# Kernel tuning notes

Hardware: AMD Instinct MI355X
Metric: run time of the kernel (lower is better)

The kernel has to match this reference:

```python
import jax, jax.numpy as jnp
import numpy as np

BATCH, SEQ, IN_DIM, OUT_DIM = 8, 512, 32, 1
D_MODEL, N_LAYERS = 512, 4
D_INNER = 2 * D_MODEL          # expand_factor=2
D_STATE = 16
D_CONV = 4
DT_RANK = (D_MODEL + 15) // 16  # ceil(d_model/16) = 32


def setup_inputs() -> dict:
    key = jax.random.key(0)
    ks = iter(jax.random.split(key, 24))
    def w(shape, fan_in):
        return jax.random.normal(next(ks), shape, jnp.float32) * (fan_in ** -0.5)
    dt = jax.random.uniform(next(ks), (N_LAYERS, D_INNER), jnp.float32, 1e-3, 0.1)
    A_log = jnp.broadcast_to(jnp.log(jnp.arange(1, D_STATE + 1, dtype=jnp.float32)),
                             (N_LAYERS, D_INNER, D_STATE)) * 1.0
    return {
        "x": jax.random.normal(next(ks), (BATCH, SEQ, IN_DIM), jnp.float32),
        "enc_w": w((D_MODEL, IN_DIM), IN_DIM),
        "enc_b": jnp.zeros((D_MODEL,), jnp.float32),
        "in_proj_w": w((N_LAYERS, 2 * D_INNER, D_MODEL), D_MODEL),
        "conv_w": w((N_LAYERS, D_INNER, 1, D_CONV), D_CONV),
        "conv_b": jnp.zeros((N_LAYERS, D_INNER), jnp.float32),
        "x_proj_w": w((N_LAYERS, DT_RANK + 2 * D_STATE, D_INNER), D_INNER),
        "dt_proj_w": w((N_LAYERS, D_INNER, DT_RANK), DT_RANK),
        "dt_proj_b": jnp.log(jnp.expm1(dt)),  # inverse softplus init
        "A_log": A_log,
        "D": jnp.ones((N_LAYERS, D_INNER), jnp.float32),
        "out_proj_w": w((N_LAYERS, D_MODEL, D_INNER), D_INNER),
        "norm_w": jnp.ones((N_LAYERS, D_MODEL), jnp.float32),
        "dec_w1": w((D_MODEL // 2, D_MODEL), D_MODEL),
        "dec_b1": jnp.zeros((D_MODEL // 2,), jnp.float32),
        "dec_w2": w((OUT_DIM, D_MODEL // 2), D_MODEL // 2),
        "dec_b2": jnp.zeros((OUT_DIM,), jnp.float32),
    }


def _rmsnorm(x, w, eps=1e-5):
    return x * jax.lax.rsqrt(jnp.mean(x * x, axis=-1, keepdims=True) + eps) * w


def _mixer(x, in_w, cw, cb, xp_w, dtp_w, dtp_b, A_log, Dp, out_w):
    B, L, _ = x.shape
    xz = x @ in_w.T                               # (B,L,2*di)
    xr, z = jnp.split(xz, 2, axis=-1)
    # causal depthwise conv1d (cross-correlation, left pad d_conv-1)
    xc = jax.lax.conv_general_dilated(
        xr.transpose(0, 2, 1), cw, window_strides=(1,),
        padding=[(D_CONV - 1, 0)], feature_group_count=D_INNER,
        dimension_numbers=("NCW", "OIW", "NCW"))    # (B,di,L)
    xr = jax.nn.silu(xc.transpose(0, 2, 1) + cb)   # (B,L,di)
    dbc = xr @ xp_w.T                              # (B,L,dt_rank+2N)
    delta = jax.nn.softplus(dbc[..., :DT_RANK] @ dtp_w.T + dtp_b)  # (B,L,di)
    Bm = dbc[..., DT_RANK:DT_RANK + D_STATE]       # (B,L,N)
    Cm = dbc[..., DT_RANK + D_STATE:]              # (B,L,N)
    A = -jnp.exp(A_log)                            # (di,N)
    dA = jnp.exp(delta[..., None] * A)             # (B,L,di,N)
    dBx = delta[..., None] * Bm[:, :, None, :] * xr[..., None]
    def step(h, inputs):
        dA_t, dBx_t = inputs
        h = dA_t * h + dBx_t
        return h, h
    h0 = jnp.zeros((B, D_INNER, D_STATE), xr.dtype)
    _, hs = jax.lax.scan(step, h0, (dA.transpose(1, 0, 2, 3), dBx.transpose(1, 0, 2, 3)))
    y = jnp.einsum("lbdn,bln->bld", hs, Cm) + Dp * xr
    y = y * jax.nn.silu(z)
    return y @ out_w.T


def reference(x, enc_w, enc_b, in_proj_w, conv_w, conv_b, x_proj_w, dt_proj_w,
              dt_proj_b, A_log, D, out_proj_w, norm_w, dec_w1, dec_b1, dec_w2, dec_b2):
    h = x @ enc_w.T + enc_b
    for i in range(in_proj_w.shape[0]):   # residual pre-norm Mamba blocks
        h = h + _mixer(_rmsnorm(h, norm_w[i]), in_proj_w[i], conv_w[i], conv_b[i],
                       x_proj_w[i], dt_proj_w[i], dt_proj_b[i], A_log[i], D[i],
                       out_proj_w[i])
    h = h[:, -1, :]
    h = jax.nn.relu(h @ dec_w1.T + dec_b1)
    return (h @ dec_w2.T + dec_b2).reshape(-1)
```

## Files before the change

### kernel.cpp

```cpp
#include <hip/hip_runtime.h>
#include <math.h>

#define BATCH   8
#define SEQ     512
#define IN_DIM  32
#define D_MODEL 512
#define N_LAYERS 4
#define D_INNER 1024
#define D_STATE 16
#define D_CONV  4
#define DT_RANK 32
#define NTOK    (BATCH * SEQ)
#define BLK_T   32
#define NCHUNK  (SEQ / BLK_T)

typedef __attribute__((ext_vector_type(8))) short short8_t;
typedef __attribute__((ext_vector_type(4))) float floatx4;

__device__ __forceinline__ float sigmoidf_(float x) { return 1.f / (1.f + __expf(-x)); }

__device__ __forceinline__ unsigned short f2bf(float f) {
    unsigned int u = __float_as_uint(f);
    return (unsigned short)((u + 0x7fffu + ((u >> 16) & 1u)) >> 16);
}
__device__ __forceinline__ float bf2f(unsigned short u) {
    return __uint_as_float((unsigned int)u << 16);
}

__global__ __launch_bounds__(256) void cast_all_kernel(
    const float* __restrict__ a, unsigned short* __restrict__ oa, int qa,
    const float* __restrict__ b, unsigned short* __restrict__ ob, int qb,
    const float* __restrict__ c, unsigned short* __restrict__ oc, int qc)
{
    int v = blockIdx.x * 256 + threadIdx.x;
    const float* in; unsigned short* out;
    if (v < qa)                { in = a; out = oa; }
    else if (v < qa + qb)      { v -= qa; in = b; out = ob; }
    else if (v < qa + qb + qc) { v -= qa + qb; in = c; out = oc; }
    else return;
    const float4 x = *(const float4*)&in[v * 4];
    ushort4 o;
    o.x = f2bf(x.x); o.y = f2bf(x.y); o.z = f2bf(x.z); o.w = f2bf(x.w);
    *(ushort4*)&out[v * 4] = o;
}

template<int BM, int BN, bool OUTBF, bool ILV>
__global__ __launch_bounds__(256) void gemm_mfma(
    const unsigned short* __restrict__ A, int lda,
    const unsigned short* __restrict__ W, int ldw,
    const float* __restrict__ R,
    void* __restrict__ Cv, int ldc,
    int K)
{
    constexpr int MT = BM / 32;
    constexpr int NT = BN / 32;
    constexpr int SA = BM / 64;
    constexpr int SB = BN / 64;
    __shared__ __align__(16) unsigned short sA[BM * 32];
    __shared__ __align__(16) unsigned short sB[BN * 32];

    const int tid  = threadIdx.x;
    const int lane = tid & 63;
    const int wave = tid >> 6;
    const int wm0  = (wave >> 1) * (BM / 2);
    const int wn0  = (wave & 1) * (BN / 2);
    const int lrow = lane & 15;
    const int m0 = blockIdx.y * BM;
    const int n0 = blockIdx.x * BN;

    const unsigned short* aptr[SA];
    const unsigned short* bptr[SB];
    #pragma unroll
    for (int s = 0; s < SA; ++s) {
        const int r = wave * (BM / 4) + s * 16 + (lane >> 2);
        const int cc = (((lane & 3) ^ ((r >> 1) & 3))) * 8;
        aptr[s] = &A[(size_t)(m0 + r) * lda + cc];
    }
    #pragma unroll
    for (int s = 0; s < SB; ++s) {
        const int r = wave * (BN / 4) + s * 16 + (lane >> 2);
        const int cc = (((lane & 3) ^ ((r >> 1) & 3))) * 8;
        bptr[s] = &W[(size_t)(n0 + r) * ldw + cc];
    }
    int aoff[MT], boff[NT];
    #pragma unroll
    for (int mt = 0; mt < MT; ++mt) {
        const int m = wm0 + mt * 16 + lrow;
        aoff[mt] = m * 32 + (((lane >> 4) ^ ((m >> 1) & 3)) * 8);
    }
    #pragma unroll
    for (int nt = 0; nt < NT; ++nt) {
        const int n = wn0 + nt * 16 + lrow;
        boff[nt] = n * 32 + (((lane >> 4) ^ ((n >> 1) & 3)) * 8);
    }

    floatx4 acc[MT][NT];
    #pragma unroll
    for (int mt = 0; mt < MT; ++mt)
        #pragma unroll
        for (int nt = 0; nt < NT; ++nt)
            acc[mt][nt] = (floatx4){0.f, 0.f, 0.f, 0.f};

    for (int k0 = 0; k0 < K; k0 += 32) {
        #pragma unroll
        for (int s = 0; s < SA; ++s)
            __builtin_amdgcn_global_load_lds(
                (const __attribute__((address_space(1))) void*)(aptr[s] + k0),
                (__attribute__((address_space(3))) void*)&sA[(wave * (BM / 4) + s * 16) * 32],
                16, 0, 0);
        #pragma unroll
        for (int s = 0; s < SB; ++s)
            __builtin_amdgcn_global_load_lds(
                (const __attribute__((address_space(1))) void*)(bptr[s] + k0),
                (__attribute__((address_space(3))) void*)&sB[(wave * (BN / 4) + s * 16) * 32],
                16, 0, 0);
        __syncthreads();
        short8_t af[MT], bfr[NT];
        #pragma unroll
        for (int mt = 0; mt < MT; ++mt)
            af[mt] = *(const short8_t*)&sA[aoff[mt]];
        #pragma unroll
        for (int nt = 0; nt < NT; ++nt)
            bfr[nt] = *(const short8_t*)&sB[boff[nt]];
        #pragma unroll
        for (int mt = 0; mt < MT; ++mt)
            #pragma unroll
            for (int nt = 0; nt < NT; ++nt)
                acc[mt][nt] = __builtin_amdgcn_mfma_f32_16x16x32_bf16(af[mt], bfr[nt], acc[mt][nt], 0, 0, 0);
        __syncthreads();
    }

    #pragma unroll
    for (int mt = 0; mt < MT; ++mt) {
        const int mbase = m0 + wm0 + mt * 16 + (lane >> 4) * 4;
        #pragma unroll
        for (int nt = 0; nt < NT; ++nt) {
            const int n = n0 + wn0 + nt * 16 + (lane & 15);
            int np = n;
            if (ILV) np = (n < 32) ? n : ((n < 48) ? 32 + 2 * (n - 32) : 33 + 2 * (n - 48));
            #pragma unroll
            for (int r = 0; r < 4; ++r) {
                float v = acc[mt][nt][r];
                if (OUTBF) {
                    ((unsigned short*)Cv)[(size_t)(mbase + r) * ldc + np] = f2bf(v);
                } else {
                    if (R) v += R[(size_t)(mbase + r) * ldc + np];
                    ((float*)Cv)[(size_t)(mbase + r) * ldc + np] = v;
                }
            }
        }
    }
}

template<bool SOFTPLUS>
__global__ __launch_bounds__(256) void gemm_bt64(
    const float* __restrict__ A, int lda,
    const float* __restrict__ W,
    const float* __restrict__ bias,
    float* __restrict__ C,
    int N, int K, int ldc)
{
    __shared__ __align__(16) float As[16][64];
    __shared__ __align__(16) float Ws[16][64];
    const int tid = threadIdx.x;
    const int tx = tid & 15, ty = tid >> 4;
    const int m0 = blockIdx.y * 64, n0 = blockIdx.x * 64;
    const int lm = tid >> 2;
    const int lk = (tid & 3) * 4;

    float acc[4][4] = {};
    for (int k0 = 0; k0 < K; k0 += 16) {
        float4 av = *(const float4*)&A[(size_t)(m0 + lm) * lda + k0 + lk];
        float4 wv = *(const float4*)&W[(size_t)(n0 + lm) * K   + k0 + lk];
        As[lk + 0][lm] = av.x; As[lk + 1][lm] = av.y; As[lk + 2][lm] = av.z; As[lk + 3][lm] = av.w;
        Ws[lk + 0][lm] = wv.x; Ws[lk + 1][lm] = wv.y; Ws[lk + 2][lm] = wv.z; Ws[lk + 3][lm] = wv.w;
        __syncthreads();
        #pragma unroll
        for (int k = 0; k < 16; ++k) {
            float4 a4 = *(const float4*)&As[k][ty * 4];
            float4 b4 = *(const float4*)&Ws[k][tx * 4];
            float a[4] = {a4.x, a4.y, a4.z, a4.w};
            float b[4] = {b4.x, b4.y, b4.z, b4.w};
            #pragma unroll
            for (int i = 0; i < 4; ++i)
                #pragma unroll
                for (int j = 0; j < 4; ++j)
                    acc[i][j] = fmaf(a[i], b[j], acc[i][j]);
        }
        __syncthreads();
    }
    #pragma unroll
    for (int i = 0; i < 4; ++i) {
        const int m = m0 + ty * 4 + i;
        #pragma unroll
        for (int j = 0; j < 4; ++j) {
            const int n = n0 + tx * 4 + j;
            float v = acc[i][j] + bias[n];
            if (SOFTPLUS) v = (v > 20.f) ? v : log1pf(__expf(v));
            C[(size_t)m * ldc + n] = v;
        }
    }
}

__global__ __launch_bounds__(256) void rmsnorm_kernel(
    const float* __restrict__ h, const float* __restrict__ w, unsigned short* __restrict__ xn)
{
    const int tok = blockIdx.x, tid = threadIdx.x;
    const float* row = h + (size_t)tok * D_MODEL;
    float v0 = row[tid], v1 = row[tid + 256];
    float s = v0 * v0 + v1 * v1;
    #pragma unroll
    for (int off = 32; off > 0; off >>= 1) s += __shfl_down(s, off, 64);
    __shared__ float ss[4];
    if ((tid & 63) == 0) ss[tid >> 6] = s;
    __syncthreads();
    const float total = ss[0] + ss[1] + ss[2] + ss[3];
    const float scale = rsqrtf(total * (1.f / (float)D_MODEL) + 1e-5f);
    unsigned short* orow = xn + (size_t)tok * D_MODEL;
    orow[tid]       = f2bf(v0 * scale * w[tid]);
    orow[tid + 256] = f2bf(v1 * scale * w[tid + 256]);
}

__global__ __launch_bounds__(256) void conv_silu_kernel(
    const unsigned short* __restrict__ xz, const float* __restrict__ cw,
    const float* __restrict__ cb, unsigned short* __restrict__ xr_bf)
{
    const int idx = blockIdx.x * 256 + threadIdx.x;
    const int d   = idx & (D_INNER - 1);
    const int tok = idx >> 10;
    const int l   = tok & (SEQ - 1);
    float acc = cb[d];
    #pragma unroll
    for (int k = 0; k < D_CONV; ++k) {
        const int t = l - (D_CONV - 1) + k;
        if (t >= 0)
            acc = fmaf(bf2f(xz[(size_t)(tok + t - l) * (2 * D_INNER) + d]), cw[d * D_CONV + k], acc);
    }
    const float v = acc * sigmoidf_(acc);
    xr_bf[(size_t)tok * D_INNER + d] = f2bf(v);
}


__global__ __launch_bounds__(256) void scan_state4(
    const float* __restrict__ dbc, const unsigned short* __restrict__ xrbf,
    const float* __restrict__ delta, const float* __restrict__ A_log,
    float* __restrict__ hend, float* __restrict__ cdend)
{
    const int tid = threadIdx.x;
    const int l = tid & 63, s = tid >> 6;
    const int b = blockIdx.y, c = blockIdx.z;
    const int d = blockIdx.x * 64 + l;
    const int base0 = b * SEQ + c * BLK_T;

    float An4[4];
    #pragma unroll
    for (int j = 0; j < 4; ++j)
        An4[j] = -__expf(A_log[(size_t)d * D_STATE + 4 * s + j]);

    float h0 = 0.f, h1 = 0.f, h2 = 0.f, h3 = 0.f, cd = 0.f;

    float4 pb0A, pb1A, pb0B, pb1B;
    float dtA, dtB;
    unsigned short xA, xB;

    #define LD_ST(S0, S1, DT, X, T)                                               \
    {                                                                             \
        const int row = base0 + (T);                                              \
        const float4* r4 = (const float4*)&dbc[(size_t)row * 64 + 32 + 8 * s];    \
        S0 = r4[0]; S1 = r4[1];                                                   \
        DT = delta[(size_t)row * D_INNER + d];                                    \
        X  = xrbf[(size_t)row * D_INNER + d];                                     \
    }
    #define STEP_ST(S0, S1, DT, X)                                                \
    {                                                                             \
        const float xf = bf2f(X);                                                 \
        const float dx = DT * xf;                                                 \
        cd += DT;                                                                 \
        h0 = fmaf(__expf(DT * An4[0]), h0, dx * S0.x);                            \
        h1 = fmaf(__expf(DT * An4[1]), h1, dx * S0.z);                            \
        h2 = fmaf(__expf(DT * An4[2]), h2, dx * S1.x);                            \
        h3 = fmaf(__expf(DT * An4[3]), h3, dx * S1.z);                            \
    }

    LD_ST(pb0A, pb1A, dtA, xA, 0);
    for (int t = 0; t < BLK_T; t += 2) {
        LD_ST(pb0B, pb1B, dtB, xB, t + 1);
        STEP_ST(pb0A, pb1A, dtA, xA);
        if (t + 2 < BLK_T) LD_ST(pb0A, pb1A, dtA, xA, t + 2);
        STEP_ST(pb0B, pb1B, dtB, xB);
    }
    #undef LD_ST
    #undef STEP_ST

    const size_t cb = (size_t)b * NCHUNK + c;
    hend[(cb * D_STATE + 4 * s + 0) * D_INNER + d] = h0;
    hend[(cb * D_STATE + 4 * s + 1) * D_INNER + d] = h1;
    hend[(cb * D_STATE + 4 * s + 2) * D_INNER + d] = h2;
    hend[(cb * D_STATE + 4 * s + 3) * D_INNER + d] = h3;
    if (s == 0) cdend[cb * D_INNER + d] = cd;
}

__global__ __launch_bounds__(256) void scan_comb(
    const float* __restrict__ A_log, const float* __restrict__ hend,
    const float* __restrict__ cdend, float* __restrict__ hstart)
{
    const int d = blockIdx.x * 256 + threadIdx.x;
    const int n = blockIdx.y, b = blockIdx.z;
    const float An = -__expf(A_log[(size_t)d * D_STATE + n]);
    float hs = 0.f;
    for (int c = 1; c < NCHUNK; ++c) {
        const size_t pb = (size_t)b * NCHUNK + (c - 1);
        hs = fmaf(__expf(cdend[pb * D_INNER + d] * An), hs,
                  hend[(pb * D_STATE + n) * D_INNER + d]);
        hstart[(((size_t)b * NCHUNK + c) * D_STATE + n) * D_INNER + d] = hs;
    }
}

__global__ __launch_bounds__(256) void scan_full16(
    const float* __restrict__ dbc, const unsigned short* __restrict__ xrbf,
    const unsigned short* __restrict__ xzbf, const float* __restrict__ delta,
    const float* __restrict__ A_log, const float* __restrict__ Dp,
    const float* __restrict__ hstart, unsigned short* __restrict__ y)
{
    const int tid = threadIdx.x;
    const int b = blockIdx.y, c = blockIdx.z;
    const int d = blockIdx.x * 256 + tid;
    const int base0 = b * SEQ + c * BLK_T;

    float An[16];
    {
        const float4* ar = (const float4*)&A_log[(size_t)d * D_STATE];
        #pragma unroll
        for (int q = 0; q < 4; ++q) {
            const float4 a4 = ar[q];
            An[4*q+0] = -__expf(a4.x); An[4*q+1] = -__expf(a4.y);
            An[4*q+2] = -__expf(a4.z); An[4*q+3] = -__expf(a4.w);
        }
    }
    const float Dd = Dp[d];

    float h[16];
    if (c == 0) {
        #pragma unroll
        for (int n = 0; n < 16; ++n) h[n] = 0.f;
    } else {
        const size_t hb = ((size_t)b * NCHUNK + c) * D_STATE;
        #pragma unroll
        for (int n = 0; n < 16; ++n) h[n] = hstart[(hb + n) * D_INNER + d];
    }

    float4 bcA[8], bcB[8];
    float dtA, dtB;
    unsigned short xA, xB, zA, zB;

    #define LD_FU(BC, DT, X, Z, T)                                                \
    {                                                                             \
        const int row = base0 + (T);                                              \
        const float4* r4 = (const float4*)&dbc[(size_t)row * 64 + 32];            \
        _Pragma("unroll")                                                         \
        for (int q = 0; q < 8; ++q) BC[q] = r4[q];                                \
        DT = delta[(size_t)row * D_INNER + d];                                    \
        X  = xrbf[(size_t)row * D_INNER + d];                                     \
        Z  = xzbf[(size_t)row * (2 * D_INNER) + D_INNER + d];                     \
    }
    #define STEP_FU(BC, DT, X, Z, T)                                              \
    {                                                                             \
        const float xf = bf2f(X);                                                 \
        const float dx = DT * xf;                                                 \
        float p = 0.f;                                                            \
        _Pragma("unroll")                                                         \
        for (int q = 0; q < 8; ++q) {                                             \
            const float4 v = BC[q];                                               \
            const float e0 = __expf(DT * An[2*q]);                                \
            h[2*q]   = fmaf(e0, h[2*q],   dx * v.x);                              \
            p = fmaf(v.y, h[2*q], p);                                             \
            const float e1 = __expf(DT * An[2*q+1]);                              \
            h[2*q+1] = fmaf(e1, h[2*q+1], dx * v.z);                              \
            p = fmaf(v.w, h[2*q+1], p);                                           \
        }                                                                         \
        const float zf = bf2f(Z);                                                 \
        const float yv = fmaf(Dd, xf, p);                                         \
        y[(size_t)(base0 + (T)) * D_INNER + d] = f2bf(yv * zf * sigmoidf_(zf));   \
    }

    LD_FU(bcA, dtA, xA, zA, 0);
    for (int t = 0; t < BLK_T; t += 2) {
        LD_FU(bcB, dtB, xB, zB, t + 1);
        STEP_FU(bcA, dtA, xA, zA, t);
        if (t + 2 < BLK_T) LD_FU(bcA, dtA, xA, zA, t + 2);
        STEP_FU(bcB, dtB, xB, zB, t + 1);
    }
    #undef LD_FU
    #undef STEP_FU
}

__global__ __launch_bounds__(256) void dec_kernel(
    const float* __restrict__ h, const float* __restrict__ w1, const float* __restrict__ b1,
    const float* __restrict__ w2, const float* __restrict__ b2, float* __restrict__ out)
{
    __shared__ __align__(16) float hr[D_MODEL];
    __shared__ float part[4];
    const int b = blockIdx.x, j = threadIdx.x;
    const float* row = h + ((size_t)(b * SEQ + SEQ - 1)) * D_MODEL;
    hr[j] = row[j];
    hr[j + 256] = row[j + 256];
    __syncthreads();
    float acc = b1[j];
    const float* wr = w1 + (size_t)j * D_MODEL;
    for (int k = 0; k < D_MODEL; k += 4) {
        const float4 wvv = *(const float4*)&wr[k];
        const float4 hv = *(const float4*)&hr[k];
        acc = fmaf(wvv.x, hv.x, acc); acc = fmaf(wvv.y, hv.y, acc);
        acc = fmaf(wvv.z, hv.z, acc); acc = fmaf(wvv.w, hv.w, acc);
    }
    float s = fmaxf(acc, 0.f) * w2[j];
    #pragma unroll
    for (int off = 32; off > 0; off >>= 1) s += __shfl_down(s, off, 64);
    if ((j & 63) == 0) part[j >> 6] = s;
    __syncthreads();
    if (j == 0) out[b] = part[0] + part[1] + part[2] + part[3] + b2[0];
}

extern "C" void kernel_launch(void* const* d_in, const int* in_sizes, int n_in,
                              void* d_out, int out_size, void* d_ws, size_t ws_size,
                              hipStream_t stream)
{
    const float* x      = (const float*)d_in[0];
    const float* enc_w  = (const float*)d_in[1];
    const float* enc_b  = (const float*)d_in[2];
    const float* in_w   = (const float*)d_in[3];
    const float* conv_w = (const float*)d_in[4];
    const float* conv_b = (const float*)d_in[5];
    const float* xp_w   = (const float*)d_in[6];
    const float* dtp_w  = (const float*)d_in[7];
    const float* dtp_b  = (const float*)d_in[8];
    const float* A_log  = (const float*)d_in[9];
    const float* Dp     = (const float*)d_in[10];
    const float* out_w  = (const float*)d_in[11];
    const float* norm_w = (const float*)d_in[12];
    const float* dec_w1 = (const float*)d_in[13];
    const float* dec_b1 = (const float*)d_in[14];
    const float* dec_w2 = (const float*)d_in[15];
    const float* dec_b2 = (const float*)d_in[16];
    float* out = (float*)d_out;

    float* ws     = (float*)d_ws;
    float* h      = ws;
    float* dbc    = h + (size_t)NTOK * D_MODEL;
    float* delta  = dbc + (size_t)NTOK * 64;
    float* hendb  = delta + (size_t)NTOK * D_INNER;
    float* hstab  = hendb + (size_t)BATCH * NCHUNK * D_STATE * D_INNER;
    float* cdendb = hstab + (size_t)BATCH * NCHUNK * D_STATE * D_INNER;
    float* wsend  = cdendb + (size_t)BATCH * NCHUNK * D_INNER;
    unsigned short* xz_bf   = (unsigned short*)(wsend);
    unsigned short* xn_bf   = xz_bf   + (size_t)NTOK * 2 * D_INNER;
    unsigned short* y_bf    = xn_bf   + (size_t)NTOK * D_MODEL;
    unsigned short* xr_bf   = y_bf    + (size_t)NTOK * D_INNER;
    unsigned short* inw_bf  = xr_bf   + (size_t)NTOK * D_INNER;
    unsigned short* outw_bf = inw_bf  + (size_t)N_LAYERS * 2 * D_INNER * D_MODEL;
    unsigned short* xpw_bf  = outw_bf + (size_t)N_LAYERS * D_MODEL * D_INNER;

    const int qa = N_LAYERS * 2 * D_INNER * D_MODEL / 4;
    const int qb = N_LAYERS * D_MODEL * D_INNER / 4;
    const int qc = N_LAYERS * 64 * D_INNER / 4;
    cast_all_kernel<<<(qa + qb + qc + 255) / 256, 256, 0, stream>>>(
        in_w, inw_bf, qa, out_w, outw_bf, qb, xp_w, xpw_bf, qc);

    gemm_bt64<false><<<dim3(D_MODEL / 64, NTOK / 64), 256, 0, stream>>>(
        x, IN_DIM, enc_w, enc_b, h, D_MODEL, IN_DIM, D_MODEL);

    for (int i = 0; i < N_LAYERS; ++i) {
        rmsnorm_kernel<<<NTOK, 256, 0, stream>>>(h, norm_w + (size_t)i * D_MODEL, xn_bf);

        gemm_mfma<128, 128, true, false><<<dim3(2 * D_INNER / 128, NTOK / 128), 256, 0, stream>>>(
            xn_bf, D_MODEL, inw_bf + (size_t)i * 2 * D_INNER * D_MODEL, D_MODEL,
            nullptr, xz_bf, 2 * D_INNER, D_MODEL);

        conv_silu_kernel<<<NTOK * D_INNER / 256, 256, 0, stream>>>(
            xz_bf, conv_w + (size_t)i * D_INNER * D_CONV, conv_b + (size_t)i * D_INNER, xr_bf);

        gemm_mfma<64, 64, false, true><<<dim3(1, NTOK / 64), 256, 0, stream>>>(
            xr_bf, D_INNER, xpw_bf + (size_t)i * 64 * D_INNER, D_INNER,
            nullptr, dbc, 64, D_INNER);

        gemm_bt64<true><<<dim3(D_INNER / 64, NTOK / 64), 256, 0, stream>>>(
            dbc, 64, dtp_w + (size_t)i * D_INNER * DT_RANK, dtp_b + (size_t)i * D_INNER,
            delta, D_INNER, DT_RANK, D_INNER);

        scan_state4<<<dim3(D_INNER / 64, BATCH, NCHUNK - 1), 256, 0, stream>>>(
            dbc, xr_bf, delta, A_log + (size_t)i * D_INNER * D_STATE,
            hendb, cdendb);

        scan_comb<<<dim3(D_INNER / 256, D_STATE, BATCH), 256, 0, stream>>>(
            A_log + (size_t)i * D_INNER * D_STATE, hendb, cdendb, hstab);

        scan_full16<<<dim3(D_INNER / 256, BATCH, NCHUNK), 256, 0, stream>>>(
            dbc, xr_bf, xz_bf, delta,
            A_log + (size_t)i * D_INNER * D_STATE, Dp + (size_t)i * D_INNER,
            hstab, y_bf);

        gemm_mfma<128, 64, false, false><<<dim3(D_MODEL / 64, NTOK / 128), 256, 0, stream>>>(
            y_bf, D_INNER, outw_bf + (size_t)i * D_MODEL * D_INNER, D_INNER,
            h, h, D_MODEL, D_INNER);
    }

    dec_kernel<<<BATCH, 256, 0, stream>>>(h, dec_w1, dec_b1, dec_w2, dec_b2, out);
}
```

Baseline: 727.8 us.

## Vectorize conv, fold chunk-combine into scan, shrink out-proj tile

The conv+SiLU kernel now handles 8 channels per thread with 16-byte bf16 loads and stores, cutting per-element load overhead. The separate scan_comb kernel is removed and each scan_full16 block instead recomputes its starting state by looping over all earlier chunk end states. This saves a launch and the hstart buffer but adds redundant work that grows with chunk index (up to 15 chunks × 16 states of loads and exps). The out-proj GEMM tile changes from 128x64 to 64x64, doubling the block count for better occupancy.

```diff
diff --git a/kernel.cpp b/kernel.cpp
--- a/kernel.cpp
+++ b/kernel.cpp
@@ -226,18 +226,35 @@
     const float* __restrict__ cb, unsigned short* __restrict__ xr_bf)
 {
     const int idx = blockIdx.x * 256 + threadIdx.x;
-    const int d   = idx & (D_INNER - 1);
-    const int tok = idx >> 10;
+    const int dq  = idx & (D_INNER / 8 - 1);
+    const int d0  = dq * 8;
+    const int tok = idx >> 7;
     const int l   = tok & (SEQ - 1);
-    float acc = cb[d];
+
+    float4 w4[8];
+    #pragma unroll
+    for (int j = 0; j < 8; ++j) w4[j] = *(const float4*)&cw[(d0 + j) * 4];
+    const float4 cb0 = *(const float4*)&cb[d0];
+    const float4 cb1 = *(const float4*)&cb[d0 + 4];
+    float acc[8] = {cb0.x, cb0.y, cb0.z, cb0.w, cb1.x, cb1.y, cb1.z, cb1.w};
+
     #pragma unroll
     for (int k = 0; k < D_CONV; ++k) {
         const int t = l - (D_CONV - 1) + k;
-        if (t >= 0)
-            acc = fmaf(bf2f(xz[(size_t)(tok + t - l) * (2 * D_INNER) + d]), cw[d * D_CONV + k], acc);
-    }
-    const float v = acc * sigmoidf_(acc);
-    xr_bf[(size_t)tok * D_INNER + d] = f2bf(v);
+        if (t >= 0) {
+            const short8_t xv = *(const short8_t*)&xz[(size_t)(tok + t - l) * (2 * D_INNER) + d0];
+            #pragma unroll
+            for (int j = 0; j < 8; ++j)
+                acc[j] = fmaf(bf2f((unsigned short)xv[j]), ((const float*)&w4[j])[k], acc[j]);
+        }
+    }
+    short8_t o;
+    #pragma unroll
+    for (int j = 0; j < 8; ++j) {
+        const float v = acc[j] * sigmoidf_(acc[j]);
+        o[j] = (short)f2bf(v);
+    }
+    *(short8_t*)&xr_bf[(size_t)tok * D_INNER + d0] = o;
 }
 
 
@@ -300,27 +317,12 @@
     if (s == 0) cdend[cb * D_INNER + d] = cd;
 }
 
-__global__ __launch_bounds__(256) void scan_comb(
-    const float* __restrict__ A_log, const float* __restrict__ hend,
-    const float* __restrict__ cdend, float* __restrict__ hstart)
-{
-    const int d = blockIdx.x * 256 + threadIdx.x;
-    const int n = blockIdx.y, b = blockIdx.z;
-    const float An = -__expf(A_log[(size_t)d * D_STATE + n]);
-    float hs = 0.f;
-    for (int c = 1; c < NCHUNK; ++c) {
-        const size_t pb = (size_t)b * NCHUNK + (c - 1);
-        hs = fmaf(__expf(cdend[pb * D_INNER + d] * An), hs,
-                  hend[(pb * D_STATE + n) * D_INNER + d]);
-        hstart[(((size_t)b * NCHUNK + c) * D_STATE + n) * D_INNER + d] = hs;
-    }
-}
-
 __global__ __launch_bounds__(256) void scan_full16(
     const float* __restrict__ dbc, const unsigned short* __restrict__ xrbf,
     const unsigned short* __restrict__ xzbf, const float* __restrict__ delta,
     const float* __restrict__ A_log, const float* __restrict__ Dp,
-    const float* __restrict__ hstart, unsigned short* __restrict__ y)
+    const float* __restrict__ hend, const float* __restrict__ cdend,
+    unsigned short* __restrict__ y)
 {
     const int tid = threadIdx.x;
     const int b = blockIdx.y, c = blockIdx.z;
@@ -340,13 +342,14 @@
     const float Dd = Dp[d];
 
     float h[16];
-    if (c == 0) {
-        #pragma unroll
-        for (int n = 0; n < 16; ++n) h[n] = 0.f;
-    } else {
-        const size_t hb = ((size_t)b * NCHUNK + c) * D_STATE;
-        #pragma unroll
-        for (int n = 0; n < 16; ++n) h[n] = hstart[(hb + n) * D_INNER + d];
+    #pragma unroll
+    for (int n = 0; n < 16; ++n) h[n] = 0.f;
+    for (int cc = 0; cc < c; ++cc) {
+        const size_t pb = (size_t)b * NCHUNK + cc;
+        const float e = cdend[pb * D_INNER + d];
+        #pragma unroll
+        for (int n = 0; n < 16; ++n)
+            h[n] = fmaf(__expf(e * An[n]), h[n], hend[(pb * D_STATE + n) * D_INNER + d]);
     }
 
     float4 bcA[8], bcB[8];
@@ -449,8 +452,7 @@
     float* dbc    = h + (size_t)NTOK * D_MODEL;
     float* delta  = dbc + (size_t)NTOK * 64;
     float* hendb  = delta + (size_t)NTOK * D_INNER;
-    float* hstab  = hendb + (size_t)BATCH * NCHUNK * D_STATE * D_INNER;
-    float* cdendb = hstab + (size_t)BATCH * NCHUNK * D_STATE * D_INNER;
+    float* cdendb = hendb + (size_t)BATCH * NCHUNK * D_STATE * D_INNER;
     float* wsend  = cdendb + (size_t)BATCH * NCHUNK * D_INNER;
     unsigned short* xz_bf   = (unsigned short*)(wsend);
     unsigned short* xn_bf   = xz_bf   + (size_t)NTOK * 2 * D_INNER;
@@ -476,7 +478,7 @@
             xn_bf, D_MODEL, inw_bf + (size_t)i * 2 * D_INNER * D_MODEL, D_MODEL,
             nullptr, xz_bf, 2 * D_INNER, D_MODEL);
 
-        conv_silu_kernel<<<NTOK * D_INNER / 256, 256, 0, stream>>>(
+        conv_silu_kernel<<<NTOK * (D_INNER / 8) / 256, 256, 0, stream>>>(
             xz_bf, conv_w + (size_t)i * D_INNER * D_CONV, conv_b + (size_t)i * D_INNER, xr_bf);
 
         gemm_mfma<64, 64, false, true><<<dim3(1, NTOK / 64), 256, 0, stream>>>(
@@ -491,15 +493,12 @@
             dbc, xr_bf, delta, A_log + (size_t)i * D_INNER * D_STATE,
             hendb, cdendb);
 
-        scan_comb<<<dim3(D_INNER / 256, D_STATE, BATCH), 256, 0, stream>>>(
-            A_log + (size_t)i * D_INNER * D_STATE, hendb, cdendb, hstab);
-
         scan_full16<<<dim3(D_INNER / 256, BATCH, NCHUNK), 256, 0, stream>>>(
             dbc, xr_bf, xz_bf, delta,
             A_log + (size_t)i * D_INNER * D_STATE, Dp + (size_t)i * D_INNER,
-            hstab, y_bf);
-
-        gemm_mfma<128, 64, false, false><<<dim3(D_MODEL / 64, NTOK / 128), 256, 0, stream>>>(
+            hendb, cdendb, y_bf);
+
+        gemm_mfma<64, 64, false, false><<<dim3(D_MODEL / 64, NTOK / 64), 256, 0, stream>>>(
             y_bf, D_INNER, outw_bf + (size_t)i * D_MODEL * D_INNER, D_INNER,
             h, h, D_MODEL, D_INNER);
     }
```

Measured after the change: 698.8 us. 4.0% less time.
